# Kernel optimization log

Hardware: AMD Instinct MI355X
Metric: run time of the kernel (lower is better)

Reference implementation:

```python
import jax, jax.numpy as jnp
import numpy as np

N = 512
H = 128
L = 4
NUM_RBF = 50
CUTOFF = 5.0
NMOL = 16
OUT = 1


def setup_inputs() -> dict:
    key = jax.random.key(0)
    ks = jax.random.split(key, 12)
    s = lambda f: 1.0 / np.sqrt(f)
    atomic_numbers = jax.random.randint(ks[0], (N,), 0, 100)
    positions = jax.random.normal(ks[1], (N, 3), dtype=jnp.float32) * 2.0
    batch = jnp.sort(jax.random.randint(ks[2], (N,), 0, NMOL))
    return {
        'atomic_numbers': atomic_numbers,
        'positions': positions,
        'batch': batch,
        'embed': jax.random.normal(ks[3], (100, H), dtype=jnp.float32) * 0.1,
        'msg_w1': jax.random.normal(ks[4], (L, H + NUM_RBF + 3, H), dtype=jnp.float32) * s(H + NUM_RBF + 3),
        'msg_b1': jnp.zeros((L, H), jnp.float32),
        'msg_w2': jax.random.normal(ks[5], (L, H, H), dtype=jnp.float32) * s(H),
        'msg_b2': jnp.zeros((L, H), jnp.float32),
        'upd_w1': jax.random.normal(ks[6], (L, 2 * H, H), dtype=jnp.float32) * s(2 * H),
        'upd_b1': jnp.zeros((L, H), jnp.float32),
        'upd_w2': jax.random.normal(ks[7], (L, H, H), dtype=jnp.float32) * s(H),
        'upd_b2': jnp.zeros((L, H), jnp.float32),
        'out_w1': jax.random.normal(ks[8], (H, H // 2), dtype=jnp.float32) * s(H),
        'out_b1': jnp.zeros((H // 2,), jnp.float32),
        'out_w2': jax.random.normal(ks[9], (H // 2, OUT), dtype=jnp.float32) * s(H // 2),
        'out_b2': jnp.zeros((OUT,), jnp.float32),
    }


def _forward(atomic_numbers, positions, batch, embed, msg_w1, msg_b1, msg_w2,
             msg_b2, upd_w1, upd_b1, upd_w2, upd_b2, out_w1, out_b1, out_w2, out_b2):
    x = embed[jnp.clip(atomic_numbers, 0, 99)]                      # [N,H]
    # all-pairs geometry: row i = source, col j = target (matches repeat_interleave/repeat)
    diff = positions[:, None, :] - positions[None, :, :]            # [N,N,3]
    dist = jnp.linalg.norm(diff, axis=-1)                           # [N,N]
    not_self = jnp.arange(N)[:, None] != jnp.arange(N)[None, :]
    valid = (dist < CUTOFF) & not_self                              # [N,N] edge mask
    dirs = diff / jnp.maximum(dist, 1e-8)[..., None]                # [N,N,3]
    # gaussian RBF: centers linspace(0, cutoff, num_rbf), width = cutoff/num_rbf
    centers = jnp.linspace(0.0, CUTOFF, NUM_RBF)
    width = CUTOFF / NUM_RBF
    rbf = jnp.exp(-(dist[..., None] - centers) ** 2 / (2.0 * width ** 2))  # [N,N,50]

    for l in range(L):
        # Linear over concat([x_j, rbf, dirs]) split by input blocks (same math)
        Wx = msg_w1[l, :H]
        Wr = msg_w1[l, H:H + NUM_RBF]
        Wd = msg_w1[l, H + NUM_RBF:]
        pre = (x @ Wx)[:, None, :] \
            + jnp.einsum('ijr,rh->ijh', rbf, Wr) \
            + jnp.einsum('ijd,dh->ijh', dirs, Wd) + msg_b1[l]       # [N,N,H]
        m = jax.nn.silu(pre) @ msg_w2[l] + msg_b2[l]                # [N,N,H]
        m = jnp.where(valid[..., None], m, 0.0)
        aggr = m.sum(axis=0)                                        # scatter-add to target j
        upd_in = jnp.concatenate([x, aggr], axis=-1)                # [N,2H]
        x = x + jax.nn.silu(upd_in @ upd_w1[l] + upd_b1[l]) @ upd_w2[l] + upd_b2[l]

    # per-molecule mean pool
    sums = jax.ops.segment_sum(x, batch, num_segments=NMOL)         # [NMOL,H]
    counts = jax.ops.segment_sum(jnp.ones((N,), x.dtype), batch, num_segments=NMOL)
    pooled = sums / jnp.maximum(counts, 1.0)[:, None]
    return jax.nn.silu(pooled @ out_w1 + out_b1) @ out_w2 + out_b2  # [NMOL,OUT]


def reference(atomic_numbers, positions, batch, embed, msg_w1, msg_b1, msg_w2,
              msg_b2, upd_w1, upd_b1, upd_w2, upd_b2, out_w1, out_b1, out_w2, out_b2):
    return _forward(atomic_numbers, positions, batch, embed, msg_w1, msg_b1, msg_w2,
                    msg_b2, upd_w1, upd_b1, upd_w2, upd_b2, out_w1, out_b1, out_w2, out_b2)
```

## Files before the change

kernel.cpp:

```cpp
#include <hip/hip_runtime.h>
#include <math.h>

#define N 512
#define H 128
#define L 4
#define NUM_RBF 50
#define NMOL 16
#define SUPER 64
#define FSTRIDE 72
#define QSPL 4

typedef __attribute__((ext_vector_type(8))) short short8;
typedef __attribute__((ext_vector_type(4))) float float4v;

__device__ __forceinline__ float silu_f(float v) {
    return v / (1.0f + __expf(-v));
}

__device__ __forceinline__ unsigned short f2bf(float f) {
    unsigned int u = __float_as_uint(f);
    unsigned int r = (u + 0x7FFFu + ((u >> 16) & 1u)) >> 16;
    return (unsigned short)r;
}

__global__ __launch_bounds__(H) void k_embed_lin(const int* __restrict__ an,
                                                 const float* __restrict__ embed,
                                                 const float* __restrict__ wx,
                                                 const float* __restrict__ b1,
                                                 float* __restrict__ x,
                                                 float* __restrict__ a) {
    int i = blockIdx.x, h = threadIdx.x;
    __shared__ float xs[H];
    int z = an[i];
    z = min(max(z, 0), 99);
    float xv = embed[z * H + h];
    x[i * H + h] = xv;
    xs[h] = xv;
    __syncthreads();
    float a0 = b1[h], a1 = 0.f, a2 = 0.f, a3 = 0.f;
#pragma unroll 8
    for (int k = 0; k < H; k += 4) {
        a0 += xs[k]     * wx[(k)     * H + h];
        a1 += xs[k + 1] * wx[(k + 1) * H + h];
        a2 += xs[k + 2] * wx[(k + 2) * H + h];
        a3 += xs[k + 3] * wx[(k + 3) * H + h];
    }
    a[i * H + h] = (a0 + a1) + (a2 + a3);
}

__global__ __launch_bounds__(256) void k_msg(const float* __restrict__ a,
                                             const float* __restrict__ pos,
                                             const float* __restrict__ wfeat,
                                             float* __restrict__ msum4,
                                             int* __restrict__ cnt4) {
    int bx = blockIdx.x;
    int j = bx >> 2;
    int q = bx & (QSPL - 1);
    int tid = threadIdx.x;
    int lane = tid & 63;
    int wv = tid >> 6;
    int nn = lane & 15;
    int quad = lane >> 4;

    __shared__ unsigned short F[SUPER * FSTRIDE];
    __shared__ float validf[SUPER];
    __shared__ int cnt_sh;

    if (tid == 0) cnt_sh = 0;

    float pjx = pos[j * 3 + 0], pjy = pos[j * 3 + 1], pjz = pos[j * 3 + 2];

    int hbase = wv * 32;
    short8 bfrag[2][2];
    for (int c = 0; c < 2; c++) {
        for (int t = 0; t < 2; t++) {
            short8 b;
            int h = hbase + 16 * t + nn;
#pragma unroll
            for (int jj = 0; jj < 8; jj++) {
                int k = c * 32 + quad * 8 + jj;
                float v = (k < NUM_RBF + 3) ? wfeat[k * H + h] : 0.0f;
                b[jj] = (short)f2bf(v);
            }
            bfrag[c][t] = b;
        }
    }

    const float DELTA = 5.0f / 49.0f;
    float pacc0 = 0.0f, pacc1 = 0.0f;

    const int SPQ = N / SUPER / QSPL;
    for (int s = q * SPQ; s < (q + 1) * SPQ; s++) {
        __syncthreads();
        {
            int il = tid >> 2;
            int kb = (tid & 3) * 16;
            int i = s * SUPER + il;
            float dx = pos[i * 3 + 0] - pjx;
            float dy = pos[i * 3 + 1] - pjy;
            float dz = pos[i * 3 + 2] - pjz;
            float d = sqrtf(dx * dx + dy * dy + dz * dz);
            float rinv = 1.0f / fmaxf(d, 1e-8f);
            unsigned short vals[16];
#pragma unroll
            for (int qq = 0; qq < 16; qq++) {
                int k = kb + qq;
                float v;
                if (k < NUM_RBF) {
                    float tt = d - (float)k * DELTA;
                    v = __expf(-50.0f * tt * tt);
                } else if (k == NUM_RBF)     v = dx * rinv;
                else if (k == NUM_RBF + 1)   v = dy * rinv;
                else if (k == NUM_RBF + 2)   v = dz * rinv;
                else                         v = 0.0f;
                vals[qq] = f2bf(v);
            }
            unsigned int* dst = (unsigned int*)&F[il * FSTRIDE + kb];
#pragma unroll
            for (int qq = 0; qq < 8; qq++)
                dst[qq] = (unsigned int)vals[2 * qq] | ((unsigned int)vals[2 * qq + 1] << 16);
            int v = (d < 5.0f) && (i != j);
            if ((tid & 3) == 0) validf[il] = (float)v;
            unsigned long long bal = __ballot(((lane & 3) == 0) && v);
            if (lane == 0) atomicAdd(&cnt_sh, __popcll(bal));
        }
        __syncthreads();

#pragma unroll
        for (int it = 0; it < SUPER / 16; it++) {
            int ibase = s * SUPER + it * 16 + quad * 4;
            float av0[4], av1[4];
#pragma unroll
            for (int r = 0; r < 4; r++) {
                av0[r] = a[(ibase + r) * H + hbase + nn];
                av1[r] = a[(ibase + r) * H + hbase + 16 + nn];
            }
            short8 afrag0 = *(const short8*)&F[(it * 16 + nn) * FSTRIDE + 0 * 32 + quad * 8];
            short8 afrag1 = *(const short8*)&F[(it * 16 + nn) * FSTRIDE + 1 * 32 + quad * 8];
            float4v acc0 = {0.0f, 0.0f, 0.0f, 0.0f};
            float4v acc1 = {0.0f, 0.0f, 0.0f, 0.0f};
            acc0 = __builtin_amdgcn_mfma_f32_16x16x32_bf16(afrag0, bfrag[0][0], acc0, 0, 0, 0);
            acc0 = __builtin_amdgcn_mfma_f32_16x16x32_bf16(afrag1, bfrag[1][0], acc0, 0, 0, 0);
            acc1 = __builtin_amdgcn_mfma_f32_16x16x32_bf16(afrag0, bfrag[0][1], acc1, 0, 0, 0);
            acc1 = __builtin_amdgcn_mfma_f32_16x16x32_bf16(afrag1, bfrag[1][1], acc1, 0, 0, 0);
            float4v vm4 = *(const float4v*)&validf[it * 16 + quad * 4];
#pragma unroll
            for (int r = 0; r < 4; r++) {
                pacc0 += vm4[r] * silu_f(acc0[r] + av0[r]);
                pacc1 += vm4[r] * silu_f(acc1[r] + av1[r]);
            }
        }
    }

    pacc0 += __shfl_xor(pacc0, 16, 64);
    pacc0 += __shfl_xor(pacc0, 32, 64);
    pacc1 += __shfl_xor(pacc1, 16, 64);
    pacc1 += __shfl_xor(pacc1, 32, 64);
    if (lane < 16) {
        msum4[(q * N + j) * H + hbase + nn]      = pacc0;
        msum4[(q * N + j) * H + hbase + 16 + nn] = pacc1;
    }
    if (tid == 0) cnt4[q * N + j] = cnt_sh;
}

__global__ __launch_bounds__(512) void k_update(const float* __restrict__ msum4,
                                                const int* __restrict__ cnt4,
                                                const float* __restrict__ w2,
                                                const float* __restrict__ b2,
                                                const float* __restrict__ u1,
                                                const float* __restrict__ ub1,
                                                const float* __restrict__ u2,
                                                const float* __restrict__ ub2,
                                                float* __restrict__ x,
                                                const float* __restrict__ wxn,
                                                const float* __restrict__ b1n,
                                                float* __restrict__ a_next) {
    int j = blockIdx.x;
    int h = threadIdx.x & 127;
    int grp = threadIdx.x >> 7;

    __shared__ float sj[H], xj[H], ag[H], hid[H], xn[H];
    __shared__ float part[4][H];

    if (grp == 0) {
        xj[h] = x[j * H + h];
    } else if (grp == 1) {
        sj[h] = msum4[j * H + h] + msum4[(N + j) * H + h]
              + msum4[(2 * N + j) * H + h] + msum4[(3 * N + j) * H + h];
    }
    int c = cnt4[j] + cnt4[N + j] + cnt4[2 * N + j] + cnt4[3 * N + j];
    __syncthreads();

    {
        float p0 = 0.f, p1 = 0.f, p2 = 0.f, p3 = 0.f;
        int k0 = grp * 32;
#pragma unroll 8
        for (int k = 0; k < 32; k += 4) {
            p0 += sj[k0 + k]     * w2[(k0 + k)     * H + h];
            p1 += sj[k0 + k + 1] * w2[(k0 + k + 1) * H + h];
            p2 += sj[k0 + k + 2] * w2[(k0 + k + 2) * H + h];
            p3 += sj[k0 + k + 3] * w2[(k0 + k + 3) * H + h];
        }
        part[grp][h] = (p0 + p1) + (p2 + p3);
    }
    __syncthreads();
    if (grp == 0) ag[h] = part[0][h] + part[1][h] + part[2][h] + part[3][h] + (float)c * b2[h];
    __syncthreads();

    {
        const float* src = (grp < 2) ? xj : ag;
        int sbase = (grp & 1) * 64;
        int k0 = grp * 64;
        float p0 = 0.f, p1 = 0.f, p2 = 0.f, p3 = 0.f;
#pragma unroll 8
        for (int k = 0; k < 64; k += 4) {
            p0 += src[sbase + k]     * u1[(k0 + k)     * H + h];
            p1 += src[sbase + k + 1] * u1[(k0 + k + 1) * H + h];
            p2 += src[sbase + k + 2] * u1[(k0 + k + 2) * H + h];
            p3 += src[sbase + k + 3] * u1[(k0 + k + 3) * H + h];
        }
        part[grp][h] = (p0 + p1) + (p2 + p3);
    }
    __syncthreads();
    if (grp == 0) hid[h] = silu_f(part[0][h] + part[1][h] + part[2][h] + part[3][h] + ub1[h]);
    __syncthreads();

    {
        float p0 = 0.f, p1 = 0.f, p2 = 0.f, p3 = 0.f;
        int k0 = grp * 32;
#pragma unroll 8
        for (int k = 0; k < 32; k += 4) {
            p0 += hid[k0 + k]     * u2[(k0 + k)     * H + h];
            p1 += hid[k0 + k + 1] * u2[(k0 + k + 1) * H + h];
            p2 += hid[k0 + k + 2] * u2[(k0 + k + 2) * H + h];
            p3 += hid[k0 + k + 3] * u2[(k0 + k + 3) * H + h];
        }
        part[grp][h] = (p0 + p1) + (p2 + p3);
    }
    __syncthreads();
    if (grp == 0) {
        float xv = xj[h] + part[0][h] + part[1][h] + part[2][h] + part[3][h] + ub2[h];
        x[j * H + h] = xv;
        xn[h] = xv;
    }

    if (a_next != nullptr) {
        __syncthreads();
        float p0 = 0.f, p1 = 0.f, p2 = 0.f, p3 = 0.f;
        int k0 = grp * 32;
#pragma unroll 8
        for (int k = 0; k < 32; k += 4) {
            p0 += xn[k0 + k]     * wxn[(k0 + k)     * H + h];
            p1 += xn[k0 + k + 1] * wxn[(k0 + k + 1) * H + h];
            p2 += xn[k0 + k + 2] * wxn[(k0 + k + 2) * H + h];
            p3 += xn[k0 + k + 3] * wxn[(k0 + k + 3) * H + h];
        }
        part[grp][h] = (p0 + p1) + (p2 + p3);
        __syncthreads();
        if (grp == 0)
            a_next[j * H + h] = part[0][h] + part[1][h] + part[2][h] + part[3][h] + b1n[h];
    }
}

__global__ __launch_bounds__(H) void k_pool(const float* __restrict__ x,
                                            const int* __restrict__ batch,
                                            const float* __restrict__ ow1,
                                            const float* __restrict__ ob1,
                                            const float* __restrict__ ow2,
                                            const float* __restrict__ ob2,
                                            float* __restrict__ out) {
    int m = blockIdx.x;
    int h = threadIdx.x;
    __shared__ int lo_s, hi_s;
    __shared__ float pooled[H];
    __shared__ float hid[H / 2];

    if (h == 0) {
        int a = 0, b = N;
        while (a < b) { int mid = (a + b) >> 1; if (batch[mid] < m) a = mid + 1; else b = mid; }
        lo_s = a;
        b = N;
        while (a < b) { int mid = (a + b) >> 1; if (batch[mid] < m + 1) a = mid + 1; else b = mid; }
        hi_s = a;
    }
    __syncthreads();

    int lo = lo_s, hi = hi_s;
    float s = 0.0f;
    for (int i = lo; i < hi; i++) s += x[i * H + h];
    pooled[h] = s / (float)max(hi - lo, 1);
    __syncthreads();

    if (h < H / 2) {
        float p0 = 0.f, p1 = 0.f;
        for (int k = 0; k < H; k += 2) {
            p0 += pooled[k]     * ow1[(k)     * (H / 2) + h];
            p1 += pooled[k + 1] * ow1[(k + 1) * (H / 2) + h];
        }
        hid[h] = silu_f(p0 + p1 + ob1[h]);
    }
    __syncthreads();

    if (h == 0) {
        float o = ob2[0];
        for (int k = 0; k < H / 2; k++) o += hid[k] * ow2[k];
        out[m] = o;
    }
}

extern "C" void kernel_launch(void* const* d_in, const int* in_sizes, int n_in,
                              void* d_out, int out_size, void* d_ws, size_t ws_size,
                              hipStream_t stream) {
    const int*   an      = (const int*)d_in[0];
    const float* pos     = (const float*)d_in[1];
    const int*   batch   = (const int*)d_in[2];
    const float* embed   = (const float*)d_in[3];
    const float* msg_w1  = (const float*)d_in[4];
    const float* msg_b1  = (const float*)d_in[5];
    const float* msg_w2  = (const float*)d_in[6];
    const float* msg_b2  = (const float*)d_in[7];
    const float* upd_w1  = (const float*)d_in[8];
    const float* upd_b1  = (const float*)d_in[9];
    const float* upd_w2  = (const float*)d_in[10];
    const float* upd_b2  = (const float*)d_in[11];
    const float* out_w1  = (const float*)d_in[12];
    const float* out_b1  = (const float*)d_in[13];
    const float* out_w2  = (const float*)d_in[14];
    const float* out_b2  = (const float*)d_in[15];
    float* out = (float*)d_out;

    float* x     = (float*)d_ws;
    float* a     = x + N * H;
    float* msum4 = a + N * H;
    int*   cnt4  = (int*)(msum4 + QSPL * N * H);

    const int W1ROWS = H + NUM_RBF + 3;

    k_embed_lin<<<N, H, 0, stream>>>(an, embed, msg_w1, msg_b1, x, a);
    for (int l = 0; l < L; l++) {
        k_msg<<<QSPL * N, 256, 0, stream>>>(a, pos, msg_w1 + l * W1ROWS * H + H * H,
                                            msum4, cnt4);
        const float* wxn = (l + 1 < L) ? (msg_w1 + (l + 1) * W1ROWS * H) : nullptr;
        const float* b1n = (l + 1 < L) ? (msg_b1 + (l + 1) * H) : nullptr;
        float* an_ = (l + 1 < L) ? a : nullptr;
        k_update<<<N, 512, 0, stream>>>(msum4, cnt4,
                                        msg_w2 + l * H * H, msg_b2 + l * H,
                                        upd_w1 + l * 2 * H * H, upd_b1 + l * H,
                                        upd_w2 + l * H * H, upd_b2 + l * H, x,
                                        wxn, b1n, an_);
    }
    k_pool<<<NMOL, H, 0, stream>>>(x, batch, out_w1, out_b1, out_w2, out_b2, out);
}
```

Measured before the change: 243.5 us.

## Build compacted neighbor lists once and iterate only valid edges in message kernel

Measured after the change: 245.4 us. About the same (+0.8%).

```diff
diff --git a/kernel.cpp b/kernel.cpp
--- a/kernel.cpp
+++ b/kernel.cpp
@@ -12,6 +12,7 @@
 
 typedef __attribute__((ext_vector_type(8))) short short8;
 typedef __attribute__((ext_vector_type(4))) float float4v;
+typedef __attribute__((ext_vector_type(4))) int int4v;
 
 __device__ __forceinline__ float silu_f(float v) {
     return v / (1.0f + __expf(-v));
@@ -23,36 +24,80 @@
     return (unsigned short)r;
 }
 
-__global__ __launch_bounds__(H) void k_embed_lin(const int* __restrict__ an,
-                                                 const float* __restrict__ embed,
-                                                 const float* __restrict__ wx,
-                                                 const float* __restrict__ b1,
-                                                 float* __restrict__ x,
-                                                 float* __restrict__ a) {
-    int i = blockIdx.x, h = threadIdx.x;
+__global__ __launch_bounds__(256) void k_embed_lin(const int* __restrict__ an,
+                                                   const float* __restrict__ embed,
+                                                   const float* __restrict__ pos,
+                                                   const float* __restrict__ wx,
+                                                   const float* __restrict__ b1,
+                                                   float* __restrict__ x,
+                                                   float* __restrict__ a,
+                                                   int* __restrict__ nbr,
+                                                   int* __restrict__ ncnt) {
+    int j = blockIdx.x;
+    int tid = threadIdx.x;
+    int lane = tid & 63;
+    int wv = tid >> 6;
+
     __shared__ float xs[H];
-    int z = an[i];
-    z = min(max(z, 0), 99);
-    float xv = embed[z * H + h];
-    x[i * H + h] = xv;
-    xs[h] = xv;
-    __syncthreads();
-    float a0 = b1[h], a1 = 0.f, a2 = 0.f, a3 = 0.f;
-#pragma unroll 8
-    for (int k = 0; k < H; k += 4) {
-        a0 += xs[k]     * wx[(k)     * H + h];
-        a1 += xs[k + 1] * wx[(k + 1) * H + h];
-        a2 += xs[k + 2] * wx[(k + 2) * H + h];
-        a3 += xs[k + 3] * wx[(k + 3) * H + h];
-    }
-    a[i * H + h] = (a0 + a1) + (a2 + a3);
+    __shared__ int wsum[4];
+
+    float pjx = pos[j * 3 + 0], pjy = pos[j * 3 + 1], pjz = pos[j * 3 + 2];
+
+    float xv = 0.0f;
+    if (tid < H) {
+        int z = an[j];
+        z = min(max(z, 0), 99);
+        xv = embed[z * H + tid];
+        xs[tid] = xv;
+    }
+
+    int total = 0;
+#pragma unroll
+    for (int r = 0; r < 2; r++) {
+        int i = r * 256 + tid;
+        float dx = pos[i * 3 + 0] - pjx;
+        float dy = pos[i * 3 + 1] - pjy;
+        float dz = pos[i * 3 + 2] - pjz;
+        float d2 = dx * dx + dy * dy + dz * dz;
+        int valid = (d2 < 25.0f) && (i != j);
+        unsigned long long m = __ballot(valid);
+        int pre = __popcll(m & ((1ull << lane) - 1ull));
+        if (lane == 0) wsum[wv] = __popcll(m);
+        __syncthreads();
+        int wbase = total;
+        for (int w = 0; w < 4; w++) {
+            if (w < wv) wbase += wsum[w];
+        }
+        int newtotal = total + wsum[0] + wsum[1] + wsum[2] + wsum[3];
+        if (valid) nbr[j * 512 + wbase + pre] = i;
+        __syncthreads();
+        total = newtotal;
+    }
+    int padded = (total + 63) & ~63;
+    for (int s = total + tid; s < padded; s += 256) nbr[j * 512 + s] = j;
+    if (tid == 0) ncnt[j] = total;
+
+    if (tid < H) {
+        int h = tid;
+        float a0 = b1[h], a1 = 0.f, a2 = 0.f, a3 = 0.f;
+#pragma unroll 8
+        for (int k = 0; k < H; k += 4) {
+            a0 += xs[k]     * wx[(k)     * H + h];
+            a1 += xs[k + 1] * wx[(k + 1) * H + h];
+            a2 += xs[k + 2] * wx[(k + 2) * H + h];
+            a3 += xs[k + 3] * wx[(k + 3) * H + h];
+        }
+        x[j * H + h] = xv;
+        a[j * H + h] = (a0 + a1) + (a2 + a3);
+    }
 }
 
 __global__ __launch_bounds__(256) void k_msg(const float* __restrict__ a,
                                              const float* __restrict__ pos,
+                                             const int* __restrict__ nbr,
+                                             const int* __restrict__ ncnt,
                                              const float* __restrict__ wfeat,
-                                             float* __restrict__ msum4,
-                                             int* __restrict__ cnt4) {
+                                             float* __restrict__ msum4) {
     int bx = blockIdx.x;
     int j = bx >> 2;
     int q = bx & (QSPL - 1);
@@ -63,11 +108,9 @@
     int quad = lane >> 4;
 
     __shared__ unsigned short F[SUPER * FSTRIDE];
-    __shared__ float validf[SUPER];
-    __shared__ int cnt_sh;
-
-    if (tid == 0) cnt_sh = 0;
-
+    __shared__ int nidx[SUPER];
+
+    int cnt = ncnt[j];
     float pjx = pos[j * 3 + 0], pjy = pos[j * 3 + 1], pjz = pos[j * 3 + 2];
 
     int hbase = wv * 32;
@@ -89,16 +132,17 @@
     const float DELTA = 5.0f / 49.0f;
     float pacc0 = 0.0f, pacc1 = 0.0f;
 
-    const int SPQ = N / SUPER / QSPL;
-    for (int s = q * SPQ; s < (q + 1) * SPQ; s++) {
+    int S = (cnt + 63) >> 6;
+    for (int s = q; s < S; s += QSPL) {
         __syncthreads();
         {
             int il = tid >> 2;
             int kb = (tid & 3) * 16;
-            int i = s * SUPER + il;
-            float dx = pos[i * 3 + 0] - pjx;
-            float dy = pos[i * 3 + 1] - pjy;
-            float dz = pos[i * 3 + 2] - pjz;
+            int ni = nbr[j * 512 + s * 64 + il];
+            if ((tid & 3) == 0) nidx[il] = ni;
+            float dx = pos[ni * 3 + 0] - pjx;
+            float dy = pos[ni * 3 + 1] - pjy;
+            float dz = pos[ni * 3 + 2] - pjz;
             float d = sqrtf(dx * dx + dy * dy + dz * dz);
             float rinv = 1.0f / fmaxf(d, 1e-8f);
             unsigned short vals[16];
@@ -119,21 +163,18 @@
 #pragma unroll
             for (int qq = 0; qq < 8; qq++)
                 dst[qq] = (unsigned int)vals[2 * qq] | ((unsigned int)vals[2 * qq + 1] << 16);
-            int v = (d < 5.0f) && (i != j);
-            if ((tid & 3) == 0) validf[il] = (float)v;
-            unsigned long long bal = __ballot(((lane & 3) == 0) && v);
-            if (lane == 0) atomicAdd(&cnt_sh, __popcll(bal));
         }
         __syncthreads();
 
 #pragma unroll
         for (int it = 0; it < SUPER / 16; it++) {
-            int ibase = s * SUPER + it * 16 + quad * 4;
+            int lbase = it * 16 + quad * 4;
+            int4v ni4 = *(const int4v*)&nidx[lbase];
             float av0[4], av1[4];
 #pragma unroll
             for (int r = 0; r < 4; r++) {
-                av0[r] = a[(ibase + r) * H + hbase + nn];
-                av1[r] = a[(ibase + r) * H + hbase + 16 + nn];
+                av0[r] = a[ni4[r] * H + hbase + nn];
+                av1[r] = a[ni4[r] * H + hbase + 16 + nn];
             }
             short8 afrag0 = *(const short8*)&F[(it * 16 + nn) * FSTRIDE + 0 * 32 + quad * 8];
             short8 afrag1 = *(const short8*)&F[(it * 16 + nn) * FSTRIDE + 1 * 32 + quad * 8];
@@ -143,11 +184,11 @@
             acc0 = __builtin_amdgcn_mfma_f32_16x16x32_bf16(afrag1, bfrag[1][0], acc0, 0, 0, 0);
             acc1 = __builtin_amdgcn_mfma_f32_16x16x32_bf16(afrag0, bfrag[0][1], acc1, 0, 0, 0);
             acc1 = __builtin_amdgcn_mfma_f32_16x16x32_bf16(afrag1, bfrag[1][1], acc1, 0, 0, 0);
-            float4v vm4 = *(const float4v*)&validf[it * 16 + quad * 4];
 #pragma unroll
             for (int r = 0; r < 4; r++) {
-                pacc0 += vm4[r] * silu_f(acc0[r] + av0[r]);
-                pacc1 += vm4[r] * silu_f(acc1[r] + av1[r]);
+                float vm = (s * 64 + lbase + r < cnt) ? 1.0f : 0.0f;
+                pacc0 += vm * silu_f(acc0[r] + av0[r]);
+                pacc1 += vm * silu_f(acc1[r] + av1[r]);
             }
         }
     }
@@ -160,11 +201,10 @@
         msum4[(q * N + j) * H + hbase + nn]      = pacc0;
         msum4[(q * N + j) * H + hbase + 16 + nn] = pacc1;
     }
-    if (tid == 0) cnt4[q * N + j] = cnt_sh;
 }
 
 __global__ __launch_bounds__(512) void k_update(const float* __restrict__ msum4,
-                                                const int* __restrict__ cnt4,
+                                                const int* __restrict__ ncnt,
                                                 const float* __restrict__ w2,
                                                 const float* __restrict__ b2,
                                                 const float* __restrict__ u1,
@@ -188,7 +228,7 @@
         sj[h] = msum4[j * H + h] + msum4[(N + j) * H + h]
               + msum4[(2 * N + j) * H + h] + msum4[(3 * N + j) * H + h];
     }
-    int c = cnt4[j] + cnt4[N + j] + cnt4[2 * N + j] + cnt4[3 * N + j];
+    int c = ncnt[j];
     __syncthreads();
 
     {
@@ -332,18 +372,19 @@
     float* x     = (float*)d_ws;
     float* a     = x + N * H;
     float* msum4 = a + N * H;
-    int*   cnt4  = (int*)(msum4 + QSPL * N * H);
+    int*   nbr   = (int*)(msum4 + QSPL * N * H);
+    int*   ncnt  = nbr + N * 512;
 
     const int W1ROWS = H + NUM_RBF + 3;
 
-    k_embed_lin<<<N, H, 0, stream>>>(an, embed, msg_w1, msg_b1, x, a);
+    k_embed_lin<<<N, 256, 0, stream>>>(an, embed, pos, msg_w1, msg_b1, x, a, nbr, ncnt);
     for (int l = 0; l < L; l++) {
-        k_msg<<<QSPL * N, 256, 0, stream>>>(a, pos, msg_w1 + l * W1ROWS * H + H * H,
-                                            msum4, cnt4);
+        k_msg<<<QSPL * N, 256, 0, stream>>>(a, pos, nbr, ncnt,
+                                            msg_w1 + l * W1ROWS * H + H * H, msum4);
         const float* wxn = (l + 1 < L) ? (msg_w1 + (l + 1) * W1ROWS * H) : nullptr;
         const float* b1n = (l + 1 < L) ? (msg_b1 + (l + 1) * H) : nullptr;
         float* an_ = (l + 1 < L) ? a : nullptr;
-        k_update<<<N, 512, 0, stream>>>(msum4, cnt4,
+        k_update<<<N, 512, 0, stream>>>(msum4, ncnt,
                                         msg_w2 + l * H * H, msg_b2 + l * H,
                                         upd_w1 + l * 2 * H * H, upd_b1 + l * H,
                                         upd_w2 + l * H * H, upd_b2 + l * H, x,
```
